# Performance work log

Hardware: AMD Instinct MI355X
Metric: run time of the kernel (lower is better)

The kernel has to match this reference:

```python
import jax, jax.numpy as jnp
import numpy as np

N, F, D, M, B, K = 100000, 256, 128, 10, 32768, 32


def setup_inputs() -> dict:
    key = jax.random.key(0)
    ks = jax.random.split(key, 14)
    stdv = float(1.0 / np.sqrt(D))
    inp = {
        "feature": jax.random.normal(ks[0], (N, F), jnp.float32),
        "flow_char_adj": jax.random.uniform(ks[1], (M, N), jnp.float32),
        "history": jax.random.randint(ks[2], (B, K), 0, N),
        "item_id": jax.random.randint(ks[3], (B,), 0, N),
        "category_r": jax.random.randint(ks[4], (B,), 0, 2),
        "category_n": jax.random.randint(ks[5], (B,), 0, 2),
        "PA_level": jax.random.randint(ks[6], (B,), 0, M),
        # learned parameters (uniform(-stdv, stdv) as in reset_parameters)
        "weight_emb": jax.random.uniform(ks[7], (F, D), jnp.float32, -stdv, stdv),
        "bias_emb": jax.random.uniform(ks[8], (D,), jnp.float32, -stdv, stdv),
        "weight_character": jax.random.uniform(ks[9], (2 * D, D), jnp.float32, -stdv, stdv),
        "att1_w": jax.random.uniform(ks[10], (D, 1), jnp.float32, -stdv, stdv),
        "att1_b": jax.random.uniform(ks[11], (1,), jnp.float32, -stdv, stdv),
        "linear1_w": jax.random.uniform(ks[12], (2 * D, D), jnp.float32, -stdv, stdv),
        "linear1_b": jax.random.uniform(ks[13], (D,), jnp.float32, -stdv, stdv),
    }
    return inp


def reference(feature, flow_char_adj, weight_emb, bias_emb, weight_character,
              att1_w, att1_b, linear1_w, linear1_b,
              history, item_id, category_r, category_n, PA_level):
    # embedding_encode
    flow_emb = feature @ weight_emb + bias_emb              # [N, D]
    character_emb = flow_char_adj @ flow_emb                # [M, D] (spmm)

    # character_modeling (shared for r and n)
    def char_lat(cat, pa):
        ce = jnp.concatenate([character_emb[cat], character_emb[pa]], axis=1)  # [B, 2D]
        return jax.nn.sigmoid(ce @ weight_character)        # [B, D]

    lat_r = char_lat(category_r, PA_level)
    lat_n = char_lat(category_n, PA_level)

    # attribute_agg: mix flow emb with its 2 category embeddings
    flow_all = (flow_emb + flow_char_adj[:2].T @ character_emb[:2]) * 0.5  # [N, D]

    # Flow_Aggregator: per-node neighbor attention (batched over ragged lists,
    # here padded to fixed degree K)
    neigh = flow_all[history]                                # [B, K, D]
    scores = neigh @ att1_w + att1_b                         # [B, K, 1]
    att = jax.nn.softmax(scores, axis=1)                     # softmax over neighbors
    agg = jnp.sum(att * neigh, axis=1)                       # [B, D]

    # NOTE: in the torch source, self_flow_latent is mutated in-place so
    # self_feats aliases neigh_feats -> both halves of the concat equal agg.
    combined = jnp.concatenate([agg, agg], axis=1)           # [B, 2D]
    out = jax.nn.relu(combined @ linear1_w + linear1_b)      # [B, D] (dropout p=0)

    pred_r = jnp.sum(lat_r * out, axis=1)                    # [B]
    pred_n = jnp.sum(lat_n * out, axis=1)                    # [B]
    return pred_r, pred_n
```

## Files before the change

### kernel.cpp

```cpp
#include <hip/hip_runtime.h>
#include <cmath>

#define NN 100000
#define FF 256
#define DDIM 128
#define MM 10
#define BB 32768
#define KK 32
#define NB1 782
#define NREP 64

#define OFF_Q     0
#define OFF_CEREP 100096
#define OFF_CE    182016
#define OFF_LAT   183296
#define OFF_CE01  185856
#define OFF_CS    186112
#define OFF_AGGB  186128
#define OFF_FE8   2283280
#define OFF_WF    5483280
#define OFF_WPF   5499664

typedef __attribute__((ext_vector_type(8))) short bf16x8;
typedef __attribute__((ext_vector_type(4))) float floatx4;
typedef __attribute__((ext_vector_type(2))) float floatx2;

__device__ __forceinline__ unsigned short f2bf(float x) {
  union { float f; unsigned u; } v; v.f = x;
  unsigned r = v.u + 0x7FFFu + ((v.u >> 16) & 1u);
  return (unsigned short)(r >> 16);
}

__device__ __forceinline__ bf16x8 cvt8(float4 a, float4 b) {
  short h[8];
  h[0] = (short)f2bf(a.x); h[1] = (short)f2bf(a.y);
  h[2] = (short)f2bf(a.z); h[3] = (short)f2bf(a.w);
  h[4] = (short)f2bf(b.x); h[5] = (short)f2bf(b.y);
  h[6] = (short)f2bf(b.z); h[7] = (short)f2bf(b.w);
  return *reinterpret_cast<bf16x8*>(h);
}

__device__ __forceinline__ void gload_lds16(const float* g, void* l) {
  __builtin_amdgcn_global_load_lds(
      (const __attribute__((address_space(1))) void*)g,
      (__attribute__((address_space(3))) void*)l, 16, 0, 0);
}

__global__ __launch_bounds__(256) void k0_wprep(const float* __restrict__ wemb,
                                                const float* __restrict__ l1w,
                                                short* __restrict__ wf,
                                                short* __restrict__ wpf)
{
  const int t = blockIdx.x * 256 + threadIdx.x;
  if (t < 4096) {
    const int kk = t >> 9, rem = t & 511;
    const int ct = rem >> 6, l = rem & 63;
    const int n = ct * 16 + (l & 15);
    const int kbase = kk * 32 + (l >> 4) * 8;
    short hi[8];
#pragma unroll
    for (int j = 0; j < 8; j++) hi[j] = (short)f2bf(wemb[(kbase + j) * 128 + n]);
    *reinterpret_cast<int4*>(&wf[((kk * 8 + ct) * 64 + l) * 8]) = *reinterpret_cast<int4*>(hi);
  } else {
    const int t2 = t - 4096;
    const int kk = t2 >> 9, rem = t2 & 511;
    const int ct = rem >> 6, l = rem & 63;
    const int n = ct * 16 + (l & 15);
    short h[8];
#pragma unroll
    for (int j = 0; j < 8; j++) {
      const int kp = kk * 32 + (l >> 4) * 8 + j;
      const int i = ((kp & 7) << 4) | (kp >> 3);
      h[j] = (short)f2bf(l1w[i * 128 + n] + l1w[(128 + i) * 128 + n]);
    }
    *reinterpret_cast<int4*>(&wpf[((kk * 8 + ct) * 64 + l) * 8]) = *reinterpret_cast<int4*>(h);
  }
}

__global__ __launch_bounds__(256, 4) void k1_fused(const float* __restrict__ feat,
    const short* __restrict__ wf, const float* __restrict__ bemb,
    const float* __restrict__ attw, const float* __restrict__ adj,
    float* __restrict__ q, unsigned char* __restrict__ fe8,
    float* __restrict__ cerep)
{
  __shared__ __align__(16) unsigned char ldsraw[34816];
  const int tid = threadIdx.x;
  const int wv = tid >> 6, l = tid & 63;
  const int lane16 = l & 15, quad = l >> 4;
  const int rowbase = blockIdx.x * 128;

  size_t gsrc[4];
#pragma unroll
  for (int i = 0; i < 4; i++) {
    int r = rowbase + wv * 32 + i * 8 + (l >> 3);
    if (r > NN - 1) r = NN - 1;
    gsrc[i] = (size_t)r * 256 + (l & 7) * 4;
  }
#pragma unroll
  for (int i = 0; i < 4; i++)
    gload_lds16(&feat[gsrc[i]], ldsraw + wv * 4096 + i * 1024);

  floatx4 acc[2][8];
#pragma unroll
  for (int rt = 0; rt < 2; rt++)
#pragma unroll
    for (int ct = 0; ct < 8; ct++) acc[rt][ct] = floatx4{0.f, 0.f, 0.f, 0.f};

#pragma unroll 2
  for (int kk = 0; kk < 8; kk++) {
    __syncthreads();
    if (kk < 7) {
      unsigned char* dst = ldsraw + ((kk + 1) & 1) * 16384 + wv * 4096;
#pragma unroll
      for (int i = 0; i < 4; i++)
        gload_lds16(&feat[gsrc[i] + (size_t)(kk + 1) * 32], dst + i * 1024);
    }
    const float* Ab = (const float*)(ldsraw + (kk & 1) * 16384);
    const short* wb = &wf[kk * 4096 + l * 8];
    bf16x8 bh[8];
#pragma unroll
    for (int ct = 0; ct < 8; ct++)
      bh[ct] = *reinterpret_cast<const bf16x8*>(&wb[ct * 512]);
    bf16x8 a[2];
#pragma unroll
    for (int rt = 0; rt < 2; rt++) {
      const int row_loc = wv * 32 + rt * 16 + lane16;
      const float4 f0 = *reinterpret_cast<const float4*>(&Ab[row_loc * 32 + quad * 8]);
      const float4 f1 = *reinterpret_cast<const float4*>(&Ab[row_loc * 32 + quad * 8 + 4]);
      a[rt] = cvt8(f0, f1);
    }
#pragma unroll
    for (int rt = 0; rt < 2; rt++)
#pragma unroll
      for (int ct = 0; ct < 8; ct++)
        acc[rt][ct] = __builtin_amdgcn_mfma_f32_16x16x32_bf16(a[rt], bh[ct], acc[rt][ct], 0, 0, 0);
  }

  float bembv[8], attwv[8];
#pragma unroll
  for (int ct = 0; ct < 8; ct++) {
    bembv[ct] = bemb[ct * 16 + lane16];
    attwv[ct] = attw[ct * 16 + lane16];
  }
#pragma unroll
  for (int rt = 0; rt < 2; rt++) {
#pragma unroll
    for (int reg = 0; reg < 4; reg++) {
      const int r = rowbase + wv * 32 + rt * 16 + quad * 4 + reg;
      float v[8]; float qp = 0.f;
#pragma unroll
      for (int ct = 0; ct < 8; ct++) {
        v[ct] = acc[rt][ct][reg] + bembv[ct];
        qp = fmaf(v[ct], attwv[ct], qp);
      }
#pragma unroll
      for (int ct = 0; ct < 8; ct++) acc[rt][ct][reg] = v[ct];
      qp += __shfl_xor(qp, 1, 16);
      qp += __shfl_xor(qp, 2, 16);
      qp += __shfl_xor(qp, 4, 16);
      qp += __shfl_xor(qp, 8, 16);
      if (r < NN) {
        unsigned u0 = __builtin_amdgcn_cvt_pk_fp8_f32(v[0], v[1], 0, false);
        u0 = __builtin_amdgcn_cvt_pk_fp8_f32(v[2], v[3], u0, true);
        unsigned u1 = __builtin_amdgcn_cvt_pk_fp8_f32(v[4], v[5], 0, false);
        u1 = __builtin_amdgcn_cvt_pk_fp8_f32(v[6], v[7], u1, true);
        *reinterpret_cast<uint2*>(&fe8[(size_t)r * 128 + lane16 * 8]) = make_uint2(u0, u1);
        if (lane16 == 0) q[r] = 0.5f * qp;
      }
    }
  }

  __syncthreads();
#pragma unroll
  for (int rt = 0; rt < 2; rt++) {
    const int rlocBase = wv * 32 + rt * 16 + quad * 4;
    const int gBase = rowbase + rlocBase;
#pragma unroll
    for (int ct = 0; ct < 8; ct++) {
      unsigned short u[4];
#pragma unroll
      for (int reg = 0; reg < 4; reg++)
        u[reg] = (gBase + reg < NN) ? f2bf(acc[rt][ct][reg]) : (unsigned short)0;
      const unsigned lo_ = (unsigned)u[0] | ((unsigned)u[1] << 16);
      const unsigned hi_ = (unsigned)u[2] | ((unsigned)u[3] << 16);
      *reinterpret_cast<uint2*>(&ldsraw[(ct * 16 + lane16) * 272 + rlocBase * 2]) =
          make_uint2(lo_, hi_);
    }
  }
  __syncthreads();

  floatx4 cacc[2];
  cacc[0] = floatx4{0.f, 0.f, 0.f, 0.f};
  cacc[1] = floatx4{0.f, 0.f, 0.f, 0.f};
  const int mclamp = (lane16 < 10) ? lane16 : 9;
#pragma unroll
  for (int kc = 0; kc < 4; kc++) {
    int n0 = rowbase + kc * 32 + quad * 8;
    if (n0 > NN - 8) n0 = NN - 8;
    const float4 f0 = *reinterpret_cast<const float4*>(&adj[(size_t)mclamp * NN + n0]);
    const float4 f1 = *reinterpret_cast<const float4*>(&adj[(size_t)mclamp * NN + n0 + 4]);
    const bf16x8 afr = cvt8(f0, f1);
#pragma unroll
    for (int tt = 0; tt < 2; tt++) {
      const int col = (wv * 2 + tt) * 16 + lane16;
      const bf16x8 bfr = *reinterpret_cast<const bf16x8*>(
          &ldsraw[col * 272 + (kc * 32 + quad * 8) * 2]);
      cacc[tt] = __builtin_amdgcn_mfma_f32_16x16x32_bf16(afr, bfr, cacc[tt], 0, 0, 0);
    }
  }
  float* myrep = &cerep[(blockIdx.x & (NREP - 1)) * 1280];
#pragma unroll
  for (int tt = 0; tt < 2; tt++) {
#pragma unroll
    for (int reg = 0; reg < 4; reg++) {
      const int m = quad * 4 + reg;
      if (m < 10)
        atomicAdd(&myrep[m * 128 + (wv * 2 + tt) * 16 + lane16], cacc[tt][reg]);
    }
  }
}

__global__ __launch_bounds__(256) void k3r_reduce(const float* __restrict__ cerep,
                                                  float* __restrict__ ce)
{
  const int o = blockIdx.x * 256 + threadIdx.x;
  if (o < 1280) {
    float s = 0.f;
#pragma unroll 8
    for (int r = 0; r < NREP; r++) s += cerep[r * 1280 + o];
    ce[o] = s;
  }
}

__global__ __launch_bounds__(128) void k3_prep(const float* __restrict__ ce,
    const float* __restrict__ wchar, const float* __restrict__ attw,
    float* __restrict__ latTab, float* __restrict__ ce01p, float* __restrict__ cs)
{
  const int blk = blockIdx.x, tid = threadIdx.x;
  __shared__ float cec[128], cep[128];
  if (blk < 20) {
    const int c = blk / 10, p = blk % 10;
    cec[tid] = ce[c * 128 + tid];
    cep[tid] = ce[p * 128 + tid];
    __syncthreads();
    float s = 0.f;
#pragma unroll 4
    for (int j = 0; j < 128; j++) {
      s = fmaf(cec[j], wchar[j * 128 + tid], s);
      s = fmaf(cep[j], wchar[(128 + j) * 128 + tid], s);
    }
    latTab[blk * 128 + tid] = 1.f / (1.f + expf(-s));
  } else {
    const float s0 = ce[tid];
    const float s1 = ce[128 + tid];
    const int pidx = (tid & 15) * 8 + (tid >> 4);
    ce01p[pidx] = s0;
    ce01p[128 + pidx] = s1;
    cec[tid] = s0 * attw[tid];
    cep[tid] = s1 * attw[tid];
    __syncthreads();
    if (tid < 64) {
      float p0 = cec[tid] + cec[tid + 64];
      float p1 = cep[tid] + cep[tid + 64];
#pragma unroll
      for (int off = 32; off >= 1; off >>= 1) {
        p0 += __shfl_xor(p0, off);
        p1 += __shfl_xor(p1, off);
      }
      if (tid == 0) { cs[0] = 0.5f * p0; cs[1] = 0.5f * p1; }
    }
  }
}

__global__ __launch_bounds__(256) void k4a_attn(const unsigned char* __restrict__ fe8,
    const float* __restrict__ q, const float* __restrict__ adj,
    const int* __restrict__ history, const float* __restrict__ cs,
    const float* __restrict__ attb_p, const float* __restrict__ ce01p,
    short* __restrict__ aggb)
{
  const int tid = threadIdx.x;
  const int lane = tid & 63;
  const int wv = tid >> 6;
  const int half = lane >> 5;
  const int t = lane & 31;
  const int b = blockIdx.x * 8 + wv * 2 + half;

  const int n_my = history[b * 32 + t];
  const float a0 = adj[n_my];
  const float a1 = adj[NN + n_my];
  const float sc = q[n_my] + a0 * cs[0] + a1 * cs[1] + attb_p[0];
  float m = sc;
#pragma unroll
  for (int off = 16; off >= 1; off >>= 1) m = fmaxf(m, __shfl_xor(m, off, 32));
  const float e = expf(sc - m);
  float sum = e;
#pragma unroll
  for (int off = 16; off >= 1; off >>= 1) sum += __shfl_xor(sum, off, 32);
  const float att = e / sum;
  float p0 = att * a0, p1 = att * a1;
#pragma unroll
  for (int off = 16; off >= 1; off >>= 1) {
    p0 += __shfl_xor(p0, off, 32);
    p1 += __shfl_xor(p1, off, 32);
  }

  float4 acc = make_float4(0.f, 0.f, 0.f, 0.f);
#pragma unroll
  for (int k = 0; k < 32; k++) {
    const int nk = __shfl(n_my, k, 32);
    const float ak = __shfl(att, k, 32);
    const unsigned u = *reinterpret_cast<const unsigned*>(&fe8[(size_t)nk * 128 + t * 4]);
    const floatx2 lo = __builtin_amdgcn_cvt_pk_f32_fp8(u, false);
    const floatx2 hi = __builtin_amdgcn_cvt_pk_f32_fp8(u, true);
    acc.x = fmaf(ak, lo[0], acc.x);
    acc.y = fmaf(ak, lo[1], acc.y);
    acc.z = fmaf(ak, hi[0], acc.z);
    acc.w = fmaf(ak, hi[1], acc.w);
  }
  const int col = t * 4;
  const float4 c0 = *reinterpret_cast<const float4*>(&ce01p[col]);
  const float4 c1 = *reinterpret_cast<const float4*>(&ce01p[128 + col]);
  const float ox = 0.5f * (acc.x + p0 * c0.x + p1 * c1.x);
  const float oy = 0.5f * (acc.y + p0 * c0.y + p1 * c1.y);
  const float oz = 0.5f * (acc.z + p0 * c0.z + p1 * c1.z);
  const float ow = 0.5f * (acc.w + p0 * c0.w + p1 * c1.w);
  const unsigned lo_ = (unsigned)f2bf(ox) | ((unsigned)f2bf(oy) << 16);
  const unsigned hi_ = (unsigned)f2bf(oz) | ((unsigned)f2bf(ow) << 16);
  *reinterpret_cast<uint2*>(&aggb[(size_t)b * 128 + col]) = make_uint2(lo_, hi_);
}

__global__ __launch_bounds__(256) void k4b_mfma(const short* __restrict__ aggb,
    const short* __restrict__ wpf, const float* __restrict__ l1b,
    const float* __restrict__ latTab,
    const int* __restrict__ cr, const int* __restrict__ cn, const int* __restrict__ pa,
    float* __restrict__ out)
{
  const int tid = threadIdx.x;
  const int wv = tid >> 6, l = tid & 63;
  const int lane16 = l & 15, quad = l >> 4;
  const int rowbase = blockIdx.x * 128 + wv * 32;
  const int r0 = rowbase + lane16;
  const int r1 = r0 + 16;

  floatx4 acc[2][8];
#pragma unroll
  for (int rt = 0; rt < 2; rt++)
#pragma unroll
    for (int ct = 0; ct < 8; ct++) acc[rt][ct] = floatx4{0.f, 0.f, 0.f, 0.f};

#pragma unroll
  for (int kk = 0; kk < 4; kk++) {
    const bf16x8 a0 = *reinterpret_cast<const bf16x8*>(&aggb[(size_t)r0 * 128 + kk * 32 + quad * 8]);
    const bf16x8 a1 = *reinterpret_cast<const bf16x8*>(&aggb[(size_t)r1 * 128 + kk * 32 + quad * 8]);
    const short* wb = &wpf[kk * 4096 + l * 8];
#pragma unroll
    for (int ct = 0; ct < 8; ct++) {
      const bf16x8 bh = *reinterpret_cast<const bf16x8*>(&wb[ct * 512]);
      acc[0][ct] = __builtin_amdgcn_mfma_f32_16x16x32_bf16(a0, bh, acc[0][ct], 0, 0, 0);
      acc[1][ct] = __builtin_amdgcn_mfma_f32_16x16x32_bf16(a1, bh, acc[1][ct], 0, 0, 0);
    }
  }

  float bb[8];
#pragma unroll
  for (int ct = 0; ct < 8; ct++) bb[ct] = l1b[ct * 16 + lane16];
#pragma unroll
  for (int rt = 0; rt < 2; rt++) {
#pragma unroll
    for (int reg = 0; reg < 4; reg++) {
      const int r = rowbase + rt * 16 + quad * 4 + reg;
      const int ir  = (cr[r] * 10 + pa[r]) * 128;
      const int in_ = (cn[r] * 10 + pa[r]) * 128;
      float pr = 0.f, pn = 0.f;
#pragma unroll
      for (int ct = 0; ct < 8; ct++) {
        const float v = fmaxf(acc[rt][ct][reg] + bb[ct], 0.f);
        pr = fmaf(v, latTab[ir  + ct * 16 + lane16], pr);
        pn = fmaf(v, latTab[in_ + ct * 16 + lane16], pn);
      }
      pr += __shfl_xor(pr, 1, 16); pr += __shfl_xor(pr, 2, 16);
      pr += __shfl_xor(pr, 4, 16); pr += __shfl_xor(pr, 8, 16);
      pn += __shfl_xor(pn, 1, 16); pn += __shfl_xor(pn, 2, 16);
      pn += __shfl_xor(pn, 4, 16); pn += __shfl_xor(pn, 8, 16);
      if (lane16 == 0) { out[r] = pr; out[BB + r] = pn; }
    }
  }
}

extern "C" void kernel_launch(void* const* d_in, const int* in_sizes, int n_in,
                              void* d_out, int out_size, void* d_ws, size_t ws_size,
                              hipStream_t stream) {
  const float* feat  = (const float*)d_in[0];
  const float* adj   = (const float*)d_in[1];
  const int*   hist  = (const int*)d_in[2];
  const int*   cr    = (const int*)d_in[4];
  const int*   cn    = (const int*)d_in[5];
  const int*   pa    = (const int*)d_in[6];
  const float* wemb  = (const float*)d_in[7];
  const float* bemb  = (const float*)d_in[8];
  const float* wchar = (const float*)d_in[9];
  const float* attw  = (const float*)d_in[10];
  const float* attb  = (const float*)d_in[11];
  const float* l1w   = (const float*)d_in[12];
  const float* l1b   = (const float*)d_in[13];
  float* out = (float*)d_out;
  float* ws  = (float*)d_ws;

  float* q     = ws + OFF_Q;
  float* cerep = ws + OFF_CEREP;
  float* ce    = ws + OFF_CE;
  float* lat   = ws + OFF_LAT;
  float* ce01p = ws + OFF_CE01;
  float* cs    = ws + OFF_CS;
  short* aggb  = (short*)(ws + OFF_AGGB);
  unsigned char* fe8 = (unsigned char*)(ws + OFF_FE8);
  short* wf    = (short*)(ws + OFF_WF);
  short* wpf   = (short*)(ws + OFF_WPF);

  hipMemsetAsync(cerep, 0, NREP * 1280 * sizeof(float), stream);
  k0_wprep<<<24, 256, 0, stream>>>(wemb, l1w, wf, wpf);
  k1_fused<<<NB1, 256, 0, stream>>>(feat, wf, bemb, attw, adj, q, fe8, cerep);
  k3r_reduce<<<5, 256, 0, stream>>>(cerep, ce);
  k3_prep<<<21, 128, 0, stream>>>(ce, wchar, attw, lat, ce01p, cs);
  k4a_attn<<<4096, 256, 0, stream>>>(fe8, q, adj, hist, cs, attb, ce01p, aggb);
  k4b_mfma<<<256, 256, 0, stream>>>(aggb, wpf, l1b, lat, cr, cn, pa, out);
}
```

Before: 268.1 us.

## Split fused embedding GEMM and character-embedding spmm into separate kernels

```diff
diff --git a/kernel.cpp b/kernel.cpp
--- a/kernel.cpp
+++ b/kernel.cpp
@@ -20,6 +20,7 @@
 #define OFF_FE8   2283280
 #define OFF_WF    5483280
 #define OFF_WPF   5499664
+#define OFF_FEBF  5507856
 
 typedef __attribute__((ext_vector_type(8))) short bf16x8;
 typedef __attribute__((ext_vector_type(4))) float floatx4;
@@ -77,13 +78,13 @@
   }
 }
 
-__global__ __launch_bounds__(256, 4) void k1_fused(const float* __restrict__ feat,
+__global__ __launch_bounds__(256, 4) void k1a_gemm(const float* __restrict__ feat,
     const short* __restrict__ wf, const float* __restrict__ bemb,
-    const float* __restrict__ attw, const float* __restrict__ adj,
+    const float* __restrict__ attw,
     float* __restrict__ q, unsigned char* __restrict__ fe8,
-    float* __restrict__ cerep)
-{
-  __shared__ __align__(16) unsigned char ldsraw[34816];
+    short* __restrict__ febf)
+{
+  __shared__ __align__(16) unsigned char ldsraw[32768];
   const int tid = threadIdx.x;
   const int wv = tid >> 6, l = tid & 63;
   const int lane16 = l & 15, quad = l >> 4;
@@ -153,8 +154,6 @@
         v[ct] = acc[rt][ct][reg] + bembv[ct];
         qp = fmaf(v[ct], attwv[ct], qp);
       }
-#pragma unroll
-      for (int ct = 0; ct < 8; ct++) acc[rt][ct][reg] = v[ct];
       qp += __shfl_xor(qp, 1, 16);
       qp += __shfl_xor(qp, 2, 16);
       qp += __shfl_xor(qp, 4, 16);
@@ -165,26 +164,42 @@
         unsigned u1 = __builtin_amdgcn_cvt_pk_fp8_f32(v[4], v[5], 0, false);
         u1 = __builtin_amdgcn_cvt_pk_fp8_f32(v[6], v[7], u1, true);
         *reinterpret_cast<uint2*>(&fe8[(size_t)r * 128 + lane16 * 8]) = make_uint2(u0, u1);
+        short hb[8];
+#pragma unroll
+        for (int ct = 0; ct < 8; ct++) hb[ct] = (short)f2bf(v[ct]);
+        *reinterpret_cast<int4*>(&febf[(size_t)r * 128 + lane16 * 8]) =
+            *reinterpret_cast<int4*>(hb);
         if (lane16 == 0) q[r] = 0.5f * qp;
       }
     }
   }
-
-  __syncthreads();
-#pragma unroll
-  for (int rt = 0; rt < 2; rt++) {
-    const int rlocBase = wv * 32 + rt * 16 + quad * 4;
-    const int gBase = rowbase + rlocBase;
-#pragma unroll
-    for (int ct = 0; ct < 8; ct++) {
-      unsigned short u[4];
-#pragma unroll
-      for (int reg = 0; reg < 4; reg++)
-        u[reg] = (gBase + reg < NN) ? f2bf(acc[rt][ct][reg]) : (unsigned short)0;
-      const unsigned lo_ = (unsigned)u[0] | ((unsigned)u[1] << 16);
-      const unsigned hi_ = (unsigned)u[2] | ((unsigned)u[3] << 16);
-      *reinterpret_cast<uint2*>(&ldsraw[(ct * 16 + lane16) * 272 + rlocBase * 2]) =
-          make_uint2(lo_, hi_);
+}
+
+__global__ __launch_bounds__(256, 4) void k1b_ce(const short* __restrict__ febf,
+    const float* __restrict__ adj, float* __restrict__ cerep)
+{
+  __shared__ __align__(16) unsigned char tile[128 * 272];
+  const int tid = threadIdx.x;
+  const int wv = tid >> 6, l = tid & 63;
+  const int lane16 = l & 15, quad = l >> 4;
+  const int rowbase = blockIdx.x * 128;
+
+  const int rp = tid & 63, cseg = tid >> 6;
+  const int g0 = rowbase + 2 * rp;
+#pragma unroll
+  for (int c8 = 0; c8 < 4; c8++) {
+    const int cb = cseg * 32 + c8 * 8;
+    int4 a = make_int4(0, 0, 0, 0), b = make_int4(0, 0, 0, 0);
+    if (g0 < NN)     a = *reinterpret_cast<const int4*>(&febf[(size_t)g0 * 128 + cb]);
+    if (g0 + 1 < NN) b = *reinterpret_cast<const int4*>(&febf[(size_t)(g0 + 1) * 128 + cb]);
+    const unsigned* au = reinterpret_cast<const unsigned*>(&a);
+    const unsigned* bu = reinterpret_cast<const unsigned*>(&b);
+#pragma unroll
+    for (int jj = 0; jj < 4; jj++) {
+      const unsigned alo = au[jj] & 0xFFFFu, ahi = au[jj] >> 16;
+      const unsigned blo = bu[jj] & 0xFFFFu, bhi = bu[jj] >> 16;
+      *reinterpret_cast<unsigned*>(&tile[(cb + 2 * jj) * 272 + rp * 4])     = alo | (blo << 16);
+      *reinterpret_cast<unsigned*>(&tile[(cb + 2 * jj + 1) * 272 + rp * 4]) = ahi | (bhi << 16);
     }
   }
   __syncthreads();
@@ -204,7 +219,7 @@
     for (int tt = 0; tt < 2; tt++) {
       const int col = (wv * 2 + tt) * 16 + lane16;
       const bf16x8 bfr = *reinterpret_cast<const bf16x8*>(
-          &ldsraw[col * 272 + (kc * 32 + quad * 8) * 2]);
+          &tile[col * 272 + (kc * 32 + quad * 8) * 2]);
       cacc[tt] = __builtin_amdgcn_mfma_f32_16x16x32_bf16(afr, bfr, cacc[tt], 0, 0, 0);
     }
   }
@@ -240,8 +255,9 @@
   __shared__ float cec[128], cep[128];
   if (blk < 20) {
     const int c = blk / 10, p = blk % 10;
-    cec[tid] = ce[c * 128 + tid];
-    cep[tid] = ce[p * 128 + tid];
+    const int pt = (tid & 15) * 8 + (tid >> 4);
+    cec[tid] = ce[c * 128 + pt];
+    cep[tid] = ce[p * 128 + pt];
     __syncthreads();
     float s = 0.f;
 #pragma unroll 4
@@ -253,11 +269,11 @@
   } else {
     const float s0 = ce[tid];
     const float s1 = ce[128 + tid];
-    const int pidx = (tid & 15) * 8 + (tid >> 4);
-    ce01p[pidx] = s0;
-    ce01p[128 + pidx] = s1;
-    cec[tid] = s0 * attw[tid];
-    cep[tid] = s1 * attw[tid];
+    ce01p[tid] = s0;
+    ce01p[128 + tid] = s1;
+    const int it = ((tid & 7) << 4) | (tid >> 3);
+    cec[tid] = s0 * attw[it];
+    cep[tid] = s1 * attw[it];
     __syncthreads();
     if (tid < 64) {
       float p0 = cec[tid] + cec[tid + 64];
@@ -416,10 +432,12 @@
   unsigned char* fe8 = (unsigned char*)(ws + OFF_FE8);
   short* wf    = (short*)(ws + OFF_WF);
   short* wpf   = (short*)(ws + OFF_WPF);
+  short* febf  = (short*)(ws + OFF_FEBF);
 
   hipMemsetAsync(cerep, 0, NREP * 1280 * sizeof(float), stream);
   k0_wprep<<<24, 256, 0, stream>>>(wemb, l1w, wf, wpf);
-  k1_fused<<<NB1, 256, 0, stream>>>(feat, wf, bemb, attw, adj, q, fe8, cerep);
+  k1a_gemm<<<NB1, 256, 0, stream>>>(feat, wf, bemb, attw, q, fe8, febf);
+  k1b_ce<<<NB1, 256, 0, stream>>>(febf, adj, cerep);
   k3r_reduce<<<5, 256, 0, stream>>>(cerep, ce);
   k3_prep<<<21, 128, 0, stream>>>(ce, wchar, attw, lat, ce01p, cs);
   k4a_attn<<<4096, 256, 0, stream>>>(fe8, q, adj, hist, cs, attb, ce01p, aggb);
```

Result: slower. 280.3 us (+4.6%).

## Fuse attention aggregation with MLP epilogue and fold small reduction/memset kernels

Applied to the files above, without the earlier changes.

```diff
diff --git a/kernel.cpp b/kernel.cpp
--- a/kernel.cpp
+++ b/kernel.cpp
@@ -12,11 +12,9 @@
 
 #define OFF_Q     0
 #define OFF_CEREP 100096
-#define OFF_CE    182016
 #define OFF_LAT   183296
 #define OFF_CE01  185856
 #define OFF_CS    186112
-#define OFF_AGGB  186128
 #define OFF_FE8   2283280
 #define OFF_WF    5483280
 #define OFF_WPF   5499664
@@ -49,9 +47,12 @@
 __global__ __launch_bounds__(256) void k0_wprep(const float* __restrict__ wemb,
                                                 const float* __restrict__ l1w,
                                                 short* __restrict__ wf,
-                                                short* __restrict__ wpf)
+                                                short* __restrict__ wpf,
+                                                float* __restrict__ cerep)
 {
   const int t = blockIdx.x * 256 + threadIdx.x;
+  for (int i = t; i < NREP * 1280; i += 24 * 256) cerep[i] = 0.f;
+
   if (t < 4096) {
     const int kk = t >> 9, rem = t & 511;
     const int ct = rem >> 6, l = rem & 63;
@@ -220,19 +221,7 @@
   }
 }
 
-__global__ __launch_bounds__(256) void k3r_reduce(const float* __restrict__ cerep,
-                                                  float* __restrict__ ce)
-{
-  const int o = blockIdx.x * 256 + threadIdx.x;
-  if (o < 1280) {
-    float s = 0.f;
-#pragma unroll 8
-    for (int r = 0; r < NREP; r++) s += cerep[r * 1280 + o];
-    ce[o] = s;
-  }
-}
-
-__global__ __launch_bounds__(128) void k3_prep(const float* __restrict__ ce,
+__global__ __launch_bounds__(128) void k3_prep(const float* __restrict__ cerep,
     const float* __restrict__ wchar, const float* __restrict__ attw,
     float* __restrict__ latTab, float* __restrict__ ce01p, float* __restrict__ cs)
 {
@@ -240,8 +229,13 @@
   __shared__ float cec[128], cep[128];
   if (blk < 20) {
     const int c = blk / 10, p = blk % 10;
-    cec[tid] = ce[c * 128 + tid];
-    cep[tid] = ce[p * 128 + tid];
+    float sc_ = 0.f, sp_ = 0.f;
+#pragma unroll 4
+    for (int r = 0; r < NREP; r++) {
+      sc_ += cerep[r * 1280 + c * 128 + tid];
+      sp_ += cerep[r * 1280 + p * 128 + tid];
+    }
+    cec[tid] = sc_; cep[tid] = sp_;
     __syncthreads();
     float s = 0.f;
 #pragma unroll 4
@@ -251,8 +245,12 @@
     }
     latTab[blk * 128 + tid] = 1.f / (1.f + expf(-s));
   } else {
-    const float s0 = ce[tid];
-    const float s1 = ce[128 + tid];
+    float s0 = 0.f, s1 = 0.f;
+#pragma unroll 4
+    for (int r = 0; r < NREP; r++) {
+      s0 += cerep[r * 1280 + tid];
+      s1 += cerep[r * 1280 + 128 + tid];
+    }
     const int pidx = (tid & 15) * 8 + (tid >> 4);
     ce01p[pidx] = s0;
     ce01p[128 + pidx] = s1;
@@ -272,118 +270,122 @@
   }
 }
 
-__global__ __launch_bounds__(256) void k4a_attn(const unsigned char* __restrict__ fe8,
+__global__ __launch_bounds__(256) void k4_fused(const unsigned char* __restrict__ fe8,
     const float* __restrict__ q, const float* __restrict__ adj,
     const int* __restrict__ history, const float* __restrict__ cs,
     const float* __restrict__ attb_p, const float* __restrict__ ce01p,
-    short* __restrict__ aggb)
+    const short* __restrict__ wpf, const float* __restrict__ l1b,
+    const float* __restrict__ latTab,
+    const int* __restrict__ cr, const int* __restrict__ cn, const int* __restrict__ pa,
+    float* __restrict__ out)
 {
+  __shared__ __align__(16) unsigned char aggT[16 * 272];
+  __shared__ float s_pr[16], s_pn[16];
   const int tid = threadIdx.x;
   const int lane = tid & 63;
   const int wv = tid >> 6;
   const int half = lane >> 5;
   const int t = lane & 31;
-  const int b = blockIdx.x * 8 + wv * 2 + half;
-
-  const int n_my = history[b * 32 + t];
-  const float a0 = adj[n_my];
-  const float a1 = adj[NN + n_my];
-  const float sc = q[n_my] + a0 * cs[0] + a1 * cs[1] + attb_p[0];
-  float m = sc;
-#pragma unroll
-  for (int off = 16; off >= 1; off >>= 1) m = fmaxf(m, __shfl_xor(m, off, 32));
-  const float e = expf(sc - m);
-  float sum = e;
-#pragma unroll
-  for (int off = 16; off >= 1; off >>= 1) sum += __shfl_xor(sum, off, 32);
-  const float att = e / sum;
-  float p0 = att * a0, p1 = att * a1;
-#pragma unroll
-  for (int off = 16; off >= 1; off >>= 1) {
-    p0 += __shfl_xor(p0, off, 32);
-    p1 += __shfl_xor(p1, off, 32);
-  }
-
-  float4 acc = make_float4(0.f, 0.f, 0.f, 0.f);
-#pragma unroll
-  for (int k = 0; k < 32; k++) {
-    const int nk = __shfl(n_my, k, 32);
-    const float ak = __shfl(att, k, 32);
-    const unsigned u = *reinterpret_cast<const unsigned*>(&fe8[(size_t)nk * 128 + t * 4]);
-    const floatx2 lo = __builtin_amdgcn_cvt_pk_f32_fp8(u, false);
-    const floatx2 hi = __builtin_amdgcn_cvt_pk_f32_fp8(u, true);
-    acc.x = fmaf(ak, lo[0], acc.x);
-    acc.y = fmaf(ak, lo[1], acc.y);
-    acc.z = fmaf(ak, hi[0], acc.z);
-    acc.w = fmaf(ak, hi[1], acc.w);
-  }
-  const int col = t * 4;
-  const float4 c0 = *reinterpret_cast<const float4*>(&ce01p[col]);
-  const float4 c1 = *reinterpret_cast<const float4*>(&ce01p[128 + col]);
-  const float ox = 0.5f * (acc.x + p0 * c0.x + p1 * c1.x);
-  const float oy = 0.5f * (acc.y + p0 * c0.y + p1 * c1.y);
-  const float oz = 0.5f * (acc.z + p0 * c0.z + p1 * c1.z);
-  const float ow = 0.5f * (acc.w + p0 * c0.w + p1 * c1.w);
-  const unsigned lo_ = (unsigned)f2bf(ox) | ((unsigned)f2bf(oy) << 16);
-  const unsigned hi_ = (unsigned)f2bf(oz) | ((unsigned)f2bf(ow) << 16);
-  *reinterpret_cast<uint2*>(&aggb[(size_t)b * 128 + col]) = make_uint2(lo_, hi_);
-}
-
-__global__ __launch_bounds__(256) void k4b_mfma(const short* __restrict__ aggb,
-    const short* __restrict__ wpf, const float* __restrict__ l1b,
-    const float* __restrict__ latTab,
-    const int* __restrict__ cr, const int* __restrict__ cn, const int* __restrict__ pa,
-    float* __restrict__ out)
-{
-  const int tid = threadIdx.x;
-  const int wv = tid >> 6, l = tid & 63;
-  const int lane16 = l & 15, quad = l >> 4;
-  const int rowbase = blockIdx.x * 128 + wv * 32;
-  const int r0 = rowbase + lane16;
-  const int r1 = r0 + 16;
-
-  floatx4 acc[2][8];
-#pragma unroll
-  for (int rt = 0; rt < 2; rt++)
-#pragma unroll
-    for (int ct = 0; ct < 8; ct++) acc[rt][ct] = floatx4{0.f, 0.f, 0.f, 0.f};
-
+  const int hw = wv * 2 + half;
+  const int bbase = blockIdx.x * 16;
+
+  if (tid < 16) { s_pr[tid] = 0.f; s_pn[tid] = 0.f; }
+
+#pragma unroll
+  for (int it = 0; it < 2; it++) {
+    const int b_loc = hw * 2 + it;
+    const int b = bbase + b_loc;
+    const int n_my = history[b * 32 + t];
+    const float a0 = adj[n_my];
+    const float a1 = adj[NN + n_my];
+    const float sc = q[n_my] + a0 * cs[0] + a1 * cs[1] + attb_p[0];
+    float m = sc;
+#pragma unroll
+    for (int off = 16; off >= 1; off >>= 1) m = fmaxf(m, __shfl_xor(m, off, 32));
+    const float e = expf(sc - m);
+    float sum = e;
+#pragma unroll
+    for (int off = 16; off >= 1; off >>= 1) sum += __shfl_xor(sum, off, 32);
+    const float att = e / sum;
+    float p0 = att * a0, p1 = att * a1;
+#pragma unroll
+    for (int off = 16; off >= 1; off >>= 1) {
+      p0 += __shfl_xor(p0, off, 32);
+      p1 += __shfl_xor(p1, off, 32);
+    }
+
+    float4 acc = make_float4(0.f, 0.f, 0.f, 0.f);
+#pragma unroll
+    for (int k = 0; k < 32; k++) {
+      const int nk = __shfl(n_my, k, 32);
+      const float ak = __shfl(att, k, 32);
+      const unsigned u = *reinterpret_cast<const unsigned*>(&fe8[(size_t)nk * 128 + t * 4]);
+      const floatx2 lo = __builtin_amdgcn_cvt_pk_f32_fp8(u, false);
+      const floatx2 hi = __builtin_amdgcn_cvt_pk_f32_fp8(u, true);
+      acc.x = fmaf(ak, lo[0], acc.x);
+      acc.y = fmaf(ak, lo[1], acc.y);
+      acc.z = fmaf(ak, hi[0], acc.z);
+      acc.w = fmaf(ak, hi[1], acc.w);
+    }
+    const int col = t * 4;
+    const float4 c0 = *reinterpret_cast<const float4*>(&ce01p[col]);
+    const float4 c1 = *reinterpret_cast<const float4*>(&ce01p[128 + col]);
+    const float ox = 0.5f * (acc.x + p0 * c0.x + p1 * c1.x);
+    const float oy = 0.5f * (acc.y + p0 * c0.y + p1 * c1.y);
+    const float oz = 0.5f * (acc.z + p0 * c0.z + p1 * c1.z);
+    const float ow = 0.5f * (acc.w + p0 * c0.w + p1 * c1.w);
+    const unsigned lo_ = (unsigned)f2bf(ox) | ((unsigned)f2bf(oy) << 16);
+    const unsigned hi_ = (unsigned)f2bf(oz) | ((unsigned)f2bf(ow) << 16);
+    *reinterpret_cast<uint2*>(&aggT[b_loc * 272 + t * 8]) = make_uint2(lo_, hi_);
+  }
+  __syncthreads();
+
+  const int lane16 = lane & 15, quad = lane >> 4;
+  floatx4 acc2[2];
+  acc2[0] = floatx4{0.f, 0.f, 0.f, 0.f};
+  acc2[1] = floatx4{0.f, 0.f, 0.f, 0.f};
 #pragma unroll
   for (int kk = 0; kk < 4; kk++) {
-    const bf16x8 a0 = *reinterpret_cast<const bf16x8*>(&aggb[(size_t)r0 * 128 + kk * 32 + quad * 8]);
-    const bf16x8 a1 = *reinterpret_cast<const bf16x8*>(&aggb[(size_t)r1 * 128 + kk * 32 + quad * 8]);
-    const short* wb = &wpf[kk * 4096 + l * 8];
-#pragma unroll
-    for (int ct = 0; ct < 8; ct++) {
-      const bf16x8 bh = *reinterpret_cast<const bf16x8*>(&wb[ct * 512]);
-      acc[0][ct] = __builtin_amdgcn_mfma_f32_16x16x32_bf16(a0, bh, acc[0][ct], 0, 0, 0);
-      acc[1][ct] = __builtin_amdgcn_mfma_f32_16x16x32_bf16(a1, bh, acc[1][ct], 0, 0, 0);
-    }
-  }
-
-  float bb[8];
-#pragma unroll
-  for (int ct = 0; ct < 8; ct++) bb[ct] = l1b[ct * 16 + lane16];
-#pragma unroll
-  for (int rt = 0; rt < 2; rt++) {
-#pragma unroll
-    for (int reg = 0; reg < 4; reg++) {
-      const int r = rowbase + rt * 16 + quad * 4 + reg;
-      const int ir  = (cr[r] * 10 + pa[r]) * 128;
-      const int in_ = (cn[r] * 10 + pa[r]) * 128;
-      float pr = 0.f, pn = 0.f;
-#pragma unroll
-      for (int ct = 0; ct < 8; ct++) {
-        const float v = fmaxf(acc[rt][ct][reg] + bb[ct], 0.f);
-        pr = fmaf(v, latTab[ir  + ct * 16 + lane16], pr);
-        pn = fmaf(v, latTab[in_ + ct * 16 + lane16], pn);
-      }
-      pr += __shfl_xor(pr, 1, 16); pr += __shfl_xor(pr, 2, 16);
-      pr += __shfl_xor(pr, 4, 16); pr += __shfl_xor(pr, 8, 16);
-      pn += __shfl_xor(pn, 1, 16); pn += __shfl_xor(pn, 2, 16);
-      pn += __shfl_xor(pn, 4, 16); pn += __shfl_xor(pn, 8, 16);
-      if (lane16 == 0) { out[r] = pr; out[BB + r] = pn; }
-    }
+    const bf16x8 a = *reinterpret_cast<const bf16x8*>(
+        &aggT[lane16 * 272 + (kk * 32 + quad * 8) * 2]);
+#pragma unroll
+    for (int c2 = 0; c2 < 2; c2++) {
+      const int ct = wv * 2 + c2;
+      const bf16x8 bh = *reinterpret_cast<const bf16x8*>(
+          &wpf[(kk * 8 + ct) * 512 + lane * 8]);
+      acc2[c2] = __builtin_amdgcn_mfma_f32_16x16x32_bf16(a, bh, acc2[c2], 0, 0, 0);
+    }
+  }
+  float bbv[2], latr[2], latn[2];
+#pragma unroll
+  for (int c2 = 0; c2 < 2; c2++) bbv[c2] = l1b[(wv * 2 + c2) * 16 + lane16];
+#pragma unroll
+  for (int reg = 0; reg < 4; reg++) {
+    const int r_loc = quad * 4 + reg;
+    const int b = bbase + r_loc;
+    const int ir  = (cr[b] * 10 + pa[b]) * 128;
+    const int in_ = (cn[b] * 10 + pa[b]) * 128;
+    float pr = 0.f, pn = 0.f;
+#pragma unroll
+    for (int c2 = 0; c2 < 2; c2++) {
+      const int col = (wv * 2 + c2) * 16 + lane16;
+      const float v = fmaxf(acc2[c2][reg] + bbv[c2], 0.f);
+      pr = fmaf(v, latTab[ir + col], pr);
+      pn = fmaf(v, latTab[in_ + col], pn);
+    }
+    pr += __shfl_xor(pr, 1, 16); pr += __shfl_xor(pr, 2, 16);
+    pr += __shfl_xor(pr, 4, 16); pr += __shfl_xor(pr, 8, 16);
+    pn += __shfl_xor(pn, 1, 16); pn += __shfl_xor(pn, 2, 16);
+    pn += __shfl_xor(pn, 4, 16); pn += __shfl_xor(pn, 8, 16);
+    if (lane16 == 0) {
+      atomicAdd(&s_pr[r_loc], pr);
+      atomicAdd(&s_pn[r_loc], pn);
+    }
+  }
+  __syncthreads();
+  if (tid < 16) {
+    out[bbase + tid] = s_pr[tid];
+    out[BB + bbase + tid] = s_pn[tid];
   }
 }
 
@@ -408,20 +410,16 @@
 
   float* q     = ws + OFF_Q;
   float* cerep = ws + OFF_CEREP;
-  float* ce    = ws + OFF_CE;
   float* lat   = ws + OFF_LAT;
   float* ce01p = ws + OFF_CE01;
   float* cs    = ws + OFF_CS;
-  short* aggb  = (short*)(ws + OFF_AGGB);
   unsigned char* fe8 = (unsigned char*)(ws + OFF_FE8);
   short* wf    = (short*)(ws + OFF_WF);
   short* wpf   = (short*)(ws + OFF_WPF);
 
-  hipMemsetAsync(cerep, 0, NREP * 1280 * sizeof(float), stream);
-  k0_wprep<<<24, 256, 0, stream>>>(wemb, l1w, wf, wpf);
+  k0_wprep<<<24, 256, 0, stream>>>(wemb, l1w, wf, wpf, cerep);
   k1_fused<<<NB1, 256, 0, stream>>>(feat, wf, bemb, attw, adj, q, fe8, cerep);
-  k3r_reduce<<<5, 256, 0, stream>>>(cerep, ce);
-  k3_prep<<<21, 128, 0, stream>>>(ce, wchar, attw, lat, ce01p, cs);
-  k4a_attn<<<4096, 256, 0, stream>>>(fe8, q, adj, hist, cs, attb, ce01p, aggb);
-  k4b_mfma<<<256, 256, 0, stream>>>(aggb, wpf, l1b, lat, cr, cn, pa, out);
-}
+  k3_prep<<<21, 128, 0, stream>>>(cerep, wchar, attw, lat, ce01p, cs);
+  k4_fused<<<2048, 256, 0, stream>>>(fe8, q, adj, hist, cs, attb, ce01p,
+                                     wpf, l1b, lat, cr, cn, pa, out);
+}
```

Result: faster. 257.7 us (-3.9%).
